# Kernel optimization log

Measured on AMD Instinct MI355X. Metric: run time of the kernel, lower is better.

## Reference

```python
import jax, jax.numpy as jnp
import numpy as np

EPS = 1e-08


def setup_inputs() -> dict:
    key = jax.random.key(0)
    k1, k2, k3 = jax.random.split(key, 3)
    B, T, IN, OUT = 32, 500, 2048, 1024
    x = jax.random.normal(k1, (B, T, IN), dtype=jnp.float32)
    # torch init: normal(mean=0, std=w_init_std*sqrt(1/input_shape))
    w = jax.random.normal(k2, (IN, OUT), dtype=jnp.float32) * np.sqrt(1.0 / IN)
    # b ~ N(1.0, 0.01), clamped >= 0
    b = jnp.clip(1.0 + 0.01 * jax.random.normal(k3, (OUT,), dtype=jnp.float32), 0.0, None)
    decay_m = jnp.array([0.6], dtype=jnp.float32)  # N(0.6, .01) clamped to [0,1]
    decay_s = jnp.array([0.9], dtype=jnp.float32)  # N(0.9, .01) clamped to [0,1]
    return {"x": x, "w": w, "b": b, "decay_m": decay_m, "decay_s": decay_s}


def reference(x, w, b, decay_m, decay_s):
    # x: [B, T, IN]; w: [IN, OUT]
    B, T, _ = x.shape
    OUT = w.shape[1]
    h = jnp.einsum('btc,cd->btd', x, w)          # [B, T, OUT]
    norm = jnp.sum(w * w, axis=0)                 # [OUT]
    dm = decay_m[0]
    ds = decay_s[0]
    inv_norm = 1.0 / (norm + EPS)
    zeros = jnp.zeros((B, OUT), dtype=x.dtype)
    # spk is never assigned a spike value in the original forward (spike_fn
    # is never applied), so it remains zero throughout.
    spk = zeros

    def step(carry, inp):
        M, S, E = carry
        E = dm * norm * (E + spk)                 # spk == 0 (faithful to source)
        M = dm * (M + inp)
        S = ds * (S + inp)
        mem = M - S - E
        mthr = mem * inv_norm - b                 # [B, OUT]
        return (M, S, E), mthr

    (_, _, _), spk_rec_t = jax.lax.scan(step, (zeros, zeros, zeros),
                                        jnp.swapaxes(h, 0, 1))  # [T, B, OUT]
    spk_rec = jnp.swapaxes(spk_rec_t, 0, 1)       # [B, T, OUT]
    loss = 0.5 * jnp.mean(spk_rec ** 2)
    return (spk_rec, loss)
```

## Files before the change

### kernel.cpp

```cpp
#include <hip/hip_runtime.h>


typedef __bf16 bf16x8 __attribute__((ext_vector_type(8)));
typedef __bf16 bf16x4 __attribute__((ext_vector_type(4)));
typedef float  f32x4  __attribute__((ext_vector_type(4)));

#define BDIM 32
#define TDIM 500
#define INDIM 2048
#define OUTDIM 1024
#define MROWS 16000
#define NCHUNK 25
#define CHLEN 20
#define OUT_ELEMS 16384000

__device__ __forceinline__ void gld_lds16(const void* g, void* l) {
    __builtin_amdgcn_global_load_lds(
        (const __attribute__((address_space(1))) unsigned int*)g,
        (__attribute__((address_space(3))) unsigned int*)l, 16, 0, 0);
}

__global__ void convert_x(const float* __restrict__ x, __bf16* __restrict__ xb) {
    size_t i = ((size_t)blockIdx.x * 256 + threadIdx.x) * 8;
    float4 a = *(const float4*)(x + i);
    float4 b = *(const float4*)(x + i + 4);
    bf16x8 o;
    o[0] = (__bf16)a.x; o[1] = (__bf16)a.y; o[2] = (__bf16)a.z; o[3] = (__bf16)a.w;
    o[4] = (__bf16)b.x; o[5] = (__bf16)b.y; o[6] = (__bf16)b.z; o[7] = (__bf16)b.w;
    *(bf16x8*)(xb + i) = o;
}

__global__ void transpose_w(const float* __restrict__ w, __bf16* __restrict__ wbt,
                            float* __restrict__ normAcc) {
    __shared__ float tile[32][33];
    __shared__ float red[8][33];
    const int tx = threadIdx.x;
    const int ty = threadIdx.y;
    const int d0 = blockIdx.x * 32;
    const int c0 = blockIdx.y * 32;
    float s = 0.f;
#pragma unroll
    for (int i = 0; i < 4; ++i) {
        int c = c0 + ty + i * 8;
        float v = w[(size_t)c * OUTDIM + d0 + tx];
        tile[ty + i * 8][tx] = v;
        s += v * v;
    }
    red[ty][tx] = s;
    __syncthreads();
#pragma unroll
    for (int i = 0; i < 4; ++i) {
        int d = d0 + ty + i * 8;
        wbt[(size_t)d * INDIM + c0 + tx] = (__bf16)tile[tx][ty + i * 8];
    }
    if (ty == 0) {
        float t = red[0][tx] + red[1][tx] + red[2][tx] + red[3][tx]
                + red[4][tx] + red[5][tx] + red[6][tx] + red[7][tx];
        atomicAdd(&normAcc[d0 + tx], t);
    }
}

__global__ __launch_bounds__(512, 2) void gemm_bf16(
    const __bf16* __restrict__ A,
    const __bf16* __restrict__ Bt,
    __bf16* __restrict__ H)
{
    constexpr int K  = INDIM;
    constexpr int NT = K / 64;
    __shared__ __align__(16) __bf16 SA[2][2][2][4096];
    __shared__ __align__(16) __bf16 SB[2][2][2][4096];

    const int tid  = threadIdx.x;
    const int wave = tid >> 6;
    const int lane = tid & 63;
    const int wm   = wave >> 2;
    const int wn   = wave & 3;

    const int orig = blockIdx.x;
    const int xcd = orig & 7, within = orig >> 3;
    const int wgid = (xcd < 4) ? (xcd * 32 + within)
                               : (128 + (xcd - 4) * 31 + within);
    const int bm = (wgid >> 2) * 256;
    const int bn = (wgid & 3) * 256;

    const int srow = lane >> 2;
    const int sseg = lane & 3;
    const int scol = (sseg ^ ((srow >> 1) & 3)) * 8;
    int ra0 = bm +       wave * 16 + srow; if (ra0 > MROWS - 1) ra0 = MROWS - 1;
    int ra1 = bm + 128 + wave * 16 + srow; if (ra1 > MROWS - 1) ra1 = MROWS - 1;
    const __bf16* pA0 = A  + (size_t)ra0 * K + scol;
    const __bf16* pA1 = A  + (size_t)ra1 * K + scol;
    const __bf16* pB0 = Bt + (size_t)(bn +       wave * 16 + srow) * K + scol;
    const __bf16* pB1 = Bt + (size_t)(bn + 128 + wave * 16 + srow) * K + scol;
    const int sdst = wave * 512;

    const int mrow = lane & 15, quad = lane >> 4;
    const int swzq = quad ^ ((mrow >> 1) & 3);
    const int rdA = (wm * 64 + mrow) * 32 + swzq * 8;
    const int rdB = (wn * 32 + mrow) * 32 + swzq * 8;

    f32x4 acc[8][4] = {};
    bf16x8 a[4][2], b[2][2];

#define STG_A(NB, HH, T1) do { const __bf16* p_ = (HH) ? pA1 : pA0;            \
        gld_lds16(p_ + (size_t)(T1) * 64,      &SA[NB][HH][0][sdst]);          \
        gld_lds16(p_ + (size_t)(T1) * 64 + 32, &SA[NB][HH][1][sdst]); } while (0)
#define STG_B(NB, HH, T1) do { const __bf16* p_ = (HH) ? pB1 : pB0;            \
        gld_lds16(p_ + (size_t)(T1) * 64,      &SB[NB][HH][0][sdst]);          \
        gld_lds16(p_ + (size_t)(T1) * 64 + 32, &SB[NB][HH][1][sdst]); } while (0)
#define RD_A(BUF, HH) do { _Pragma("unroll")                                   \
        for (int i = 0; i < 4; ++i) {                                          \
            a[i][0] = *(const bf16x8*)&SA[BUF][HH][0][rdA + i * 512];          \
            a[i][1] = *(const bf16x8*)&SA[BUF][HH][1][rdA + i * 512]; } } while (0)
#define RD_B(BUF, HH) do { _Pragma("unroll")                                   \
        for (int j = 0; j < 2; ++j) {                                          \
            b[j][0] = *(const bf16x8*)&SB[BUF][HH][0][rdB + j * 512];          \
            b[j][1] = *(const bf16x8*)&SB[BUF][HH][1][rdB + j * 512]; } } while (0)
#define MM(HM, HN) do { __builtin_amdgcn_s_setprio(1);                         \
        _Pragma("unroll")                                                      \
        for (int i = 0; i < 4; ++i)                                            \
        _Pragma("unroll")                                                      \
        for (int j = 0; j < 2; ++j) {                                          \
            acc[(HM)*4+i][(HN)*2+j] = __builtin_amdgcn_mfma_f32_16x16x32_bf16( \
                a[i][0], b[j][0], acc[(HM)*4+i][(HN)*2+j], 0, 0, 0);           \
            acc[(HM)*4+i][(HN)*2+j] = __builtin_amdgcn_mfma_f32_16x16x32_bf16( \
                a[i][1], b[j][1], acc[(HM)*4+i][(HN)*2+j], 0, 0, 0); }         \
        __builtin_amdgcn_s_setprio(0); } while (0)

#define TILE(T, CUR, NB) do {                                                  \
        const bool st_   = (T) + 1 < NT;                                       \
        const bool last_ = (T) == NT - 1;                                      \
                                                           \
        RD_A(CUR, 0); RD_B(CUR, 0);                                            \
        if (st_) STG_A(NB, 0, (T) + 1);                                        \
        if (!last_) asm volatile("s_waitcnt vmcnt(4)" ::: "memory");           \
        else        asm volatile("s_waitcnt vmcnt(2)" ::: "memory");           \
        asm volatile("s_barrier" ::: "memory");                                \
        MM(0, 0);                                                              \
                                                  \
        RD_B(CUR, 1);                                                          \
        if (st_) STG_B(NB, 0, (T) + 1);                                        \
        if (!last_) asm volatile("s_waitcnt vmcnt(4)" ::: "memory");           \
        else        asm volatile("s_waitcnt vmcnt(0)" ::: "memory");           \
        asm volatile("s_barrier" ::: "memory");                                \
        MM(0, 1);                                                              \
                                                  \
        RD_A(CUR, 1);                                                          \
        if (st_) STG_B(NB, 1, (T) + 1);                                        \
        asm volatile("s_barrier" ::: "memory");                                \
        MM(1, 1);                                                              \
                                              \
        RD_B(CUR, 0);                                                          \
        if (st_) STG_A(NB, 1, (T) + 1);                                        \
        if (st_) asm volatile("s_waitcnt vmcnt(4)" ::: "memory");              \
        asm volatile("s_barrier" ::: "memory");                                \
        MM(1, 0);                                                              \
    } while (0)

    STG_A(0, 0, 0); STG_B(0, 0, 0); STG_B(0, 1, 0); STG_A(0, 1, 0);
    asm volatile("s_waitcnt vmcnt(4)" ::: "memory");
    asm volatile("s_barrier" ::: "memory");

#pragma unroll 1
    for (int tt = 0; tt < NT; tt += 2) {
        TILE(tt,     0, 1);
        TILE(tt + 1, 1, 0);
    }
#undef TILE
#undef MM
#undef RD_B
#undef RD_A
#undef STG_B
#undef STG_A

#pragma unroll
    for (int hm = 0; hm < 2; ++hm)
#pragma unroll
        for (int i = 0; i < 4; ++i)
#pragma unroll
            for (int hn = 0; hn < 2; ++hn)
#pragma unroll
                for (int j = 0; j < 2; ++j)
#pragma unroll
                    for (int r = 0; r < 4; ++r) {
                        const int R = bm + hm * 128 + wm * 64 + i * 16 + quad * 4 + r;
                        const int C = bn + hn * 128 + wn * 32 + j * 16 + mrow;
                        if (R < MROWS)
                            H[(size_t)R * OUTDIM + C] = (__bf16)acc[hm * 4 + i][hn * 2 + j][r];
                    }
}

__global__ void scan1(const __bf16* __restrict__ H,
                      f32x4* __restrict__ cM, f32x4* __restrict__ cS,
                      const float* __restrict__ dmp, const float* __restrict__ dsp) {
    const float dm = *dmp, ds = *dsp;
    const int c = blockIdx.x, b = blockIdx.y, tid = threadIdx.x;
    f32x4 M = {}, S = {};
    const __bf16* p = H + ((size_t)b * TDIM + c * CHLEN) * OUTDIM + tid * 4;
#pragma unroll 4
    for (int t = 0; t < CHLEN; ++t) {
        bf16x4 hv = *(const bf16x4*)(p + (size_t)t * OUTDIM);
        f32x4 h; h[0] = hv[0]; h[1] = hv[1]; h[2] = hv[2]; h[3] = hv[3];
        M = dm * (M + h);
        S = ds * (S + h);
    }
    const size_t idx = ((size_t)c * BDIM + b) * 256 + tid;
    cM[idx] = M;
    cS[idx] = S;
}

__global__ void scan2(float* __restrict__ cM, float* __restrict__ cS,
                      const float* __restrict__ dmp, const float* __restrict__ dsp) {
    const float dm = *dmp, ds = *dsp;
    float km = 1.f, ks = 1.f;
#pragma unroll
    for (int i = 0; i < CHLEN; ++i) { km *= dm; ks *= ds; }
    const int gid = blockIdx.x * 256 + threadIdx.x;
    const int b = gid >> 10, d = gid & 1023;
    float tM = 0.f, tS = 0.f;
    for (int c = 0; c < NCHUNK; ++c) {
        const size_t idx = (((size_t)c * BDIM + b) << 10) + d;
        float oM = cM[idx], oS = cS[idx];
        cM[idx] = tM; cS[idx] = tS;
        tM = km * tM + oM;
        tS = ks * tS + oS;
    }
}

__global__ void scan3(const __bf16* __restrict__ H,
                      const f32x4* __restrict__ cM, const f32x4* __restrict__ cS,
                      const float* __restrict__ normAcc, const float* __restrict__ bias,
                      const float* __restrict__ dmp, const float* __restrict__ dsp,
                      float* __restrict__ out, float* __restrict__ lossAcc,
                      unsigned* __restrict__ ticket) {
    const float dm = *dmp, ds = *dsp;
    const int c = blockIdx.x, b = blockIdx.y, tid = threadIdx.x;
    const size_t cidx = ((size_t)c * BDIM + b) * 256 + tid;
    f32x4 M = cM[cidx];
    f32x4 S = cS[cidx];
    f32x4 nv = *(const f32x4*)(normAcc + tid * 4);
    f32x4 inv;
    inv[0] = 1.f / (nv[0] + 1e-8f); inv[1] = 1.f / (nv[1] + 1e-8f);
    inv[2] = 1.f / (nv[2] + 1e-8f); inv[3] = 1.f / (nv[3] + 1e-8f);
    f32x4 bv = *(const f32x4*)(bias + tid * 4);

    const size_t rowbase = ((size_t)b * TDIM + c * CHLEN) * OUTDIM + tid * 4;
    const __bf16* p = H + rowbase;
    float* o = out + rowbase;
    float loss = 0.f;
#pragma unroll 4
    for (int t = 0; t < CHLEN; ++t) {
        bf16x4 hv = *(const bf16x4*)(p + (size_t)t * OUTDIM);
        f32x4 h; h[0] = hv[0]; h[1] = hv[1]; h[2] = hv[2]; h[3] = hv[3];
        M = dm * (M + h);
        S = ds * (S + h);
        f32x4 r = (M - S) * inv - bv;
        *(f32x4*)(o + (size_t)t * OUTDIM) = r;
        loss += r[0] * r[0] + r[1] * r[1] + r[2] * r[2] + r[3] * r[3];
    }
    __shared__ float red[256];
    red[tid] = loss;
    __syncthreads();
    for (int s = 128; s > 0; s >>= 1) {
        if (tid < s) red[tid] += red[tid + s];
        __syncthreads();
    }
    if (tid == 0) {
        atomicAdd(lossAcc, red[0]);
        __threadfence();
        unsigned t = atomicAdd(ticket, 1u);
        if (t == NCHUNK * BDIM - 1) {
            float total = atomicAdd(lossAcc, 0.0f);
            out[OUT_ELEMS] = 0.5f * total / (float)OUT_ELEMS;
        }
    }
}

#define OFF_H      ((size_t)0)
#define OFF_WBT    ((size_t)32768000)
#define OFF_NORM   ((size_t)36962304)
#define OFF_LOSS   ((size_t)36966400)
#define OFF_TICKET ((size_t)36966404)
#define OFF_CM     ((size_t)36966656)
#define OFF_CS     ((size_t)40243456)

extern "C" void kernel_launch(void* const* d_in, const int* in_sizes, int n_in,
                              void* d_out, int out_size, void* d_ws, size_t ws_size,
                              hipStream_t stream) {
    const float* x  = (const float*)d_in[0];
    const float* w  = (const float*)d_in[1];
    const float* bb = (const float*)d_in[2];
    const float* dm = (const float*)d_in[3];
    const float* ds = (const float*)d_in[4];

    char* ws = (char*)d_ws;
    __bf16*   H    = (__bf16*)(ws + OFF_H);
    __bf16*   WBT  = (__bf16*)(ws + OFF_WBT);
    float*    NORM = (float*)(ws + OFF_NORM);
    float*    LOSS = (float*)(ws + OFF_LOSS);
    unsigned* TICK = (unsigned*)(ws + OFF_TICKET);
    f32x4*    CM   = (f32x4*)(ws + OFF_CM);
    f32x4*    CS   = (f32x4*)(ws + OFF_CS);
    __bf16*   XB   = (__bf16*)d_out;
    float*    out  = (float*)d_out;

    hipMemsetAsync(ws + OFF_NORM, 0, 4096 + 256, stream);

    convert_x<<<16000, 256, 0, stream>>>(x, XB);
    transpose_w<<<dim3(32, 64), dim3(32, 8), 0, stream>>>(w, WBT, NORM);
    gemm_bf16<<<252, 512, 0, stream>>>(XB, WBT, H);
    scan1<<<dim3(NCHUNK, BDIM), 256, 0, stream>>>(H, CM, CS, dm, ds);
    scan2<<<128, 256, 0, stream>>>((float*)CM, (float*)CS, dm, ds);
    scan3<<<dim3(NCHUNK, BDIM), 256, 0, stream>>>(H, CM, CS, NORM, bb, dm, ds,
                                                  out, LOSS, TICK);
}
```

Before: 333.8 us.

## Load GEMM B operand directly from global into registers, dropping LDS staging

The B (weight) tile is no longer staged through shared memory. Each wave loads its own B fragments straight from global memory into double-buffered register sets that are prefetched one K-tile ahead, while A keeps its LDS double buffer. The per-tile schedule goes from four barriers to one. This removes LDS traffic and barriers for B, but adds register pressure from the extra fragment buffers and drops the cross-wave sharing of B, so each wave issues more global loads.

```diff
diff --git a/kernel.cpp b/kernel.cpp
--- a/kernel.cpp
+++ b/kernel.cpp
@@ -68,7 +68,6 @@
     constexpr int K  = INDIM;
     constexpr int NT = K / 64;
     __shared__ __align__(16) __bf16 SA[2][2][2][4096];
-    __shared__ __align__(16) __bf16 SB[2][2][2][4096];
 
     const int tid  = threadIdx.x;
     const int wave = tid >> 6;
@@ -88,89 +87,81 @@
     const int scol = (sseg ^ ((srow >> 1) & 3)) * 8;
     int ra0 = bm +       wave * 16 + srow; if (ra0 > MROWS - 1) ra0 = MROWS - 1;
     int ra1 = bm + 128 + wave * 16 + srow; if (ra1 > MROWS - 1) ra1 = MROWS - 1;
-    const __bf16* pA0 = A  + (size_t)ra0 * K + scol;
-    const __bf16* pA1 = A  + (size_t)ra1 * K + scol;
-    const __bf16* pB0 = Bt + (size_t)(bn +       wave * 16 + srow) * K + scol;
-    const __bf16* pB1 = Bt + (size_t)(bn + 128 + wave * 16 + srow) * K + scol;
+    const __bf16* pA0 = A + (size_t)ra0 * K + scol;
+    const __bf16* pA1 = A + (size_t)ra1 * K + scol;
     const int sdst = wave * 512;
 
     const int mrow = lane & 15, quad = lane >> 4;
     const int swzq = quad ^ ((mrow >> 1) & 3);
     const int rdA = (wm * 64 + mrow) * 32 + swzq * 8;
-    const int rdB = (wn * 32 + mrow) * 32 + swzq * 8;
+
+    const __bf16* pB[2][2];
+#pragma unroll
+    for (int hn = 0; hn < 2; ++hn)
+#pragma unroll
+        for (int j = 0; j < 2; ++j)
+            pB[hn][j] = Bt + (size_t)(bn + hn * 128 + wn * 32 + j * 16 + mrow) * K
+                           + quad * 8;
 
     f32x4 acc[8][4] = {};
-    bf16x8 a[4][2], b[2][2];
-
-#define STG_A(NB, HH, T1) do { const __bf16* p_ = (HH) ? pA1 : pA0;            \
-        gld_lds16(p_ + (size_t)(T1) * 64,      &SA[NB][HH][0][sdst]);          \
-        gld_lds16(p_ + (size_t)(T1) * 64 + 32, &SA[NB][HH][1][sdst]); } while (0)
-#define STG_B(NB, HH, T1) do { const __bf16* p_ = (HH) ? pB1 : pB0;            \
-        gld_lds16(p_ + (size_t)(T1) * 64,      &SB[NB][HH][0][sdst]);          \
-        gld_lds16(p_ + (size_t)(T1) * 64 + 32, &SB[NB][HH][1][sdst]); } while (0)
+    bf16x8 a[4][2];
+    bf16x8 bU[2][2][2], bL[2][2][2];
+
+#define STG_A(NB, T1) do {                                                     \
+        gld_lds16(pA0 + (size_t)(T1) * 64,      &SA[NB][0][0][sdst]);          \
+        gld_lds16(pA0 + (size_t)(T1) * 64 + 32, &SA[NB][0][1][sdst]);          \
+        gld_lds16(pA1 + (size_t)(T1) * 64,      &SA[NB][1][0][sdst]);          \
+        gld_lds16(pA1 + (size_t)(T1) * 64 + 32, &SA[NB][1][1][sdst]); } while (0)
 #define RD_A(BUF, HH) do { _Pragma("unroll")                                   \
         for (int i = 0; i < 4; ++i) {                                          \
             a[i][0] = *(const bf16x8*)&SA[BUF][HH][0][rdA + i * 512];          \
             a[i][1] = *(const bf16x8*)&SA[BUF][HH][1][rdA + i * 512]; } } while (0)
-#define RD_B(BUF, HH) do { _Pragma("unroll")                                   \
+#define BLD(SET, T1) do { _Pragma("unroll")                                    \
+        for (int hn = 0; hn < 2; ++hn) _Pragma("unroll")                       \
         for (int j = 0; j < 2; ++j) {                                          \
-            b[j][0] = *(const bf16x8*)&SB[BUF][HH][0][rdB + j * 512];          \
-            b[j][1] = *(const bf16x8*)&SB[BUF][HH][1][rdB + j * 512]; } } while (0)
-#define MM(HM, HN) do { __builtin_amdgcn_s_setprio(1);                         \
+            const __bf16* p_ = pB[hn][j] + (size_t)(T1) * 64;                  \
+            SET[hn][j][0] = *(const bf16x8*)(p_);                              \
+            SET[hn][j][1] = *(const bf16x8*)(p_ + 32); } } while (0)
+#define MM(HM, HN, SET) do { __builtin_amdgcn_s_setprio(1);                    \
         _Pragma("unroll")                                                      \
-        for (int i = 0; i < 4; ++i)                                            \
-        _Pragma("unroll")                                                      \
+        for (int i = 0; i < 4; ++i) _Pragma("unroll")                          \
         for (int j = 0; j < 2; ++j) {                                          \
             acc[(HM)*4+i][(HN)*2+j] = __builtin_amdgcn_mfma_f32_16x16x32_bf16( \
-                a[i][0], b[j][0], acc[(HM)*4+i][(HN)*2+j], 0, 0, 0);           \
+                a[i][0], SET[HN][j][0], acc[(HM)*4+i][(HN)*2+j], 0, 0, 0);     \
             acc[(HM)*4+i][(HN)*2+j] = __builtin_amdgcn_mfma_f32_16x16x32_bf16( \
-                a[i][1], b[j][1], acc[(HM)*4+i][(HN)*2+j], 0, 0, 0); }         \
+                a[i][1], SET[HN][j][1], acc[(HM)*4+i][(HN)*2+j], 0, 0, 0); }   \
         __builtin_amdgcn_s_setprio(0); } while (0)
 
-#define TILE(T, CUR, NB) do {                                                  \
-        const bool st_   = (T) + 1 < NT;                                       \
-        const bool last_ = (T) == NT - 1;                                      \
-                                                           \
-        RD_A(CUR, 0); RD_B(CUR, 0);                                            \
-        if (st_) STG_A(NB, 0, (T) + 1);                                        \
-        if (!last_) asm volatile("s_waitcnt vmcnt(4)" ::: "memory");           \
-        else        asm volatile("s_waitcnt vmcnt(2)" ::: "memory");           \
-        asm volatile("s_barrier" ::: "memory");                                \
-        MM(0, 0);                                                              \
-                                                  \
-        RD_B(CUR, 1);                                                          \
-        if (st_) STG_B(NB, 0, (T) + 1);                                        \
-        if (!last_) asm volatile("s_waitcnt vmcnt(4)" ::: "memory");           \
-        else        asm volatile("s_waitcnt vmcnt(0)" ::: "memory");           \
-        asm volatile("s_barrier" ::: "memory");                                \
-        MM(0, 1);                                                              \
-                                                  \
+#define TILE(T, CUR, BU, BL) do {                                              \
+        const bool st_ = (T) + 1 < NT;                                         \
+        RD_A(CUR, 0);                                                          \
+        if (st_) STG_A(1 - (CUR), (T) + 1);                                    \
+        if (st_) asm volatile("s_waitcnt vmcnt(4)" ::: "memory");              \
+        else     asm volatile("s_waitcnt vmcnt(0)" ::: "memory");              \
+        MM(0, 0, BU); MM(0, 1, BU);                                            \
         RD_A(CUR, 1);                                                          \
-        if (st_) STG_B(NB, 1, (T) + 1);                                        \
-        asm volatile("s_barrier" ::: "memory");                                \
-        MM(1, 1);                                                              \
-                                              \
-        RD_B(CUR, 0);                                                          \
-        if (st_) STG_A(NB, 1, (T) + 1);                                        \
-        if (st_) asm volatile("s_waitcnt vmcnt(4)" ::: "memory");              \
-        asm volatile("s_barrier" ::: "memory");                                \
-        MM(1, 0);                                                              \
+        if (st_) BLD(BL, (T) + 1);                                             \
+        MM(1, 0, BU); MM(1, 1, BU);                                            \
+        if (st_) {                                                             \
+            asm volatile("s_waitcnt vmcnt(8)" ::: "memory");                   \
+            asm volatile("s_barrier" ::: "memory");                            \
+        }                                                                      \
     } while (0)
 
-    STG_A(0, 0, 0); STG_B(0, 0, 0); STG_B(0, 1, 0); STG_A(0, 1, 0);
-    asm volatile("s_waitcnt vmcnt(4)" ::: "memory");
+    STG_A(0, 0);
+    BLD(bU, 0);
+    asm volatile("s_waitcnt vmcnt(8)" ::: "memory");
     asm volatile("s_barrier" ::: "memory");
 
 #pragma unroll 1
     for (int tt = 0; tt < NT; tt += 2) {
-        TILE(tt,     0, 1);
-        TILE(tt + 1, 1, 0);
+        TILE(tt,     0, bU, bL);
+        TILE(tt + 1, 1, bL, bU);
     }
 #undef TILE
 #undef MM
-#undef RD_B
+#undef BLD
 #undef RD_A
-#undef STG_B
 #undef STG_A
 
 #pragma unroll
```

After: 357.0 us. 7.0% more time.
